# Kernel tuning notes

Measured on AMD Instinct MI355X. Metric: run time of the kernel, lower is better.

## Reference

```python
import jax, jax.numpy as jnp
import numpy as np

B, C, CW = 64, 862, 512
F_BINS = CW // 2 + 1          # 257 rfft bins -> embedding in_features
D_MODEL, N_HEADS, D_FF, N_LAYERS = 256, 16, 512, 3
EPS = 1e-5


def setup_inputs() -> dict:
    key = jax.random.key(0)
    ks = jax.random.split(key, 12)
    s = 0.02
    return {
        'x_re': jax.random.normal(ks[0], (B, C, F_BINS), jnp.float32),
        'x_im': jax.random.normal(ks[1], (B, C, F_BINS), jnp.float32),
        # complex embedding Linear(F_BINS, D_MODEL): weight [D_MODEL, F_BINS], bias [D_MODEL]
        'emb_Wre': jax.random.normal(ks[2], (D_MODEL, F_BINS), jnp.float32) * s,
        'emb_Wim': jax.random.normal(ks[3], (D_MODEL, F_BINS), jnp.float32) * s,
        'emb_bre': jax.random.normal(ks[4], (D_MODEL,), jnp.float32) * s,
        'emb_bim': jax.random.normal(ks[5], (D_MODEL,), jnp.float32) * s,
        # per-layer FFN weights (stacked over layers)
        'W1': jax.random.normal(ks[6], (N_LAYERS, D_FF, D_MODEL), jnp.float32) * s,
        'b1': jnp.zeros((N_LAYERS, D_FF), jnp.float32),
        'W2': jax.random.normal(ks[7], (N_LAYERS, D_MODEL, D_FF), jnp.float32) * s,
        'b2': jnp.zeros((N_LAYERS, D_MODEL), jnp.float32),
        # per-layer BatchNorm affine params (attn norm and ffn norm)
        'gamma1': jnp.ones((N_LAYERS, D_MODEL), jnp.float32),
        'beta1': jnp.zeros((N_LAYERS, D_MODEL), jnp.float32),
        'gamma2': jnp.ones((N_LAYERS, D_MODEL), jnp.float32),
        'beta2': jnp.zeros((N_LAYERS, D_MODEL), jnp.float32),
    }


def _batchnorm(x, g, b):
    # Transpose(1,2) + BatchNorm1d(d_model) + Transpose(1,2): normalize each
    # feature (last axis) over (batch, seq) with batch statistics (training mode).
    m = x.mean(axis=(0, 1))
    v = x.var(axis=(0, 1))  # biased, matching torch normalization
    return (x - m) * jax.lax.rsqrt(v + EPS) * g + b


def _encoder_layer(y, Wff1, bff1, Wff2, bff2, g1, be1, g2, be2):
    # y: [2b, c, d] -- real half stacked over imag half along dim 0
    scale = float(D_MODEL // N_HEADS) ** -0.5
    b = y.shape[0] // 2
    # _MultiheadAttention: q = src, k = flip(src, dims=[1,2]), v = src (no projections applied)
    k = jnp.flip(y, axis=(1, 2))
    q_re, q_im = y[:b], y[b:]
    k_re, k_im = k[:b], k[b:]
    v_re = y[:b]
    v_im = y[:b]  # faithful to source: both halves use v[:bs//2]
    asr = scale * (q_re * k_re - q_im * k_im)
    asi = scale * (q_re * k_im - q_im * k_re)  # minus, as written in source
    o_re = asr * v_re - asi * v_im
    o_im = asr * v_im + asi * v_re
    out = jnp.concatenate([o_re, o_im], axis=0)  # [2b, c, d]
    # transpose(1,2).contiguous().view(bs, -1, d_model): a data shuffle, kept faithfully
    out = jnp.swapaxes(out, 1, 2).reshape(out.shape[0], out.shape[1], out.shape[2])
    src = y + out                       # residual (dropout = 0)
    src = _batchnorm(src, g1, be1)      # post-norm (pre_norm=False)
    ff = jnp.einsum('bcd,fd->bcf', src, Wff1) + bff1
    ff = jax.nn.gelu(ff, approximate=False)
    ff = jnp.einsum('bcf,df->bcd', ff, Wff2) + bff2
    src = src + ff
    src = _batchnorm(src, g2, be2)
    return src


def reference(x_re, x_im, emb_Wre, emb_Wim, emb_bre, emb_bim,
              W1, b1, W2, b2, gamma1, beta1, gamma2, beta2):
    # complex Linear embedding: (x_re + i x_im) @ (Wre + i Wim)^T + (bre + i bim)
    y_re = x_re @ emb_Wre.T - x_im @ emb_Wim.T + emb_bre
    y_im = x_re @ emb_Wim.T + x_im @ emb_Wre.T + emb_bim
    y = jnp.concatenate([y_re, y_im], axis=0)  # [2b, c, d_model]
    for i in range(N_LAYERS):
        y = _encoder_layer(y, W1[i], b1[i], W2[i], b2[i],
                           gamma1[i], beta1[i], gamma2[i], beta2[i])
    b = x_re.shape[0]
    # torch.view_as_complex(stack([y[:b], y[b:]], -1)) -> return real/imag stacked
    return jnp.stack([y[:b], y[b:]], axis=-1)  # [b, c, d_model, 2]
```

## Files before the change

kernel.cpp:

```cpp
#include <hip/hip_runtime.h>
#include <hip/hip_bf16.h>
#include <math.h>

#define BB   64
#define CC   862
#define FB   257
#define DM   256
#define DFF  512
#define NIMG 128
#define ROWS_RE (BB*CC)
#define ROWS_ALL (NIMG*CC)
#define NELEM ((long)ROWS_ALL*DM)

typedef __bf16 bf16x8 __attribute__((ext_vector_type(8)));
typedef float  f32x4  __attribute__((ext_vector_type(4)));

__global__ __launch_bounds__(256) void k_wcvt(const float* __restrict__ W1,
                                              const float* __restrict__ W2,
                                              __bf16* __restrict__ W1b,
                                              __bf16* __restrict__ W2b) {
  long i = ((long)blockIdx.x * 256 + threadIdx.x) * 4;
  const long N1 = 3L * DFF * DM;
  const float* src;
  __bf16* dst;
  if (i < N1) { src = W1 + i; dst = W1b + i; }
  else        { src = W2 + (i - N1); dst = W2b + (i - N1); }
  float4 x = *(const float4*)src;
  dst[0] = (__bf16)x.x; dst[1] = (__bf16)x.y;
  dst[2] = (__bf16)x.z; dst[3] = (__bf16)x.w;
}

__global__ void k_init(double* __restrict__ stats, float* __restrict__ ss) {
  int t = threadIdx.x;
  stats[t] = 0.0;
  if (t < 256) { ss[t] = 1.0f; ss[DM + t] = 0.0f; }
}

#define KE 544
#define PE 552

__global__ __launch_bounds__(256) void k_wemb(const float* __restrict__ Wre,
                                              const float* __restrict__ Wim,
                                              __bf16* __restrict__ Wb) {
  int n = blockIdx.x;
  int d = n & 255;
  bool im = (n >= 256);
  const float* Wa = im ? Wim : Wre;
  const float* Wc = im ? Wre : Wim;
  float sgn = im ? 1.0f : -1.0f;
  for (int k = threadIdx.x; k < KE; k += 256) {
    float v;
    if (k < 257)      v = Wa[(long)d * FB + k];
    else if (k < 514) v = sgn * Wc[(long)d * FB + (k - 257)];
    else              v = 0.0f;
    Wb[(long)n * KE + k] = (__bf16)v;
  }
}

__global__ __launch_bounds__(256, 4) void k_embm(
    const float* __restrict__ xr, const float* __restrict__ xi,
    const __bf16* __restrict__ Wb,
    const float* __restrict__ bre, const float* __restrict__ bim,
    float* __restrict__ A) {
  __shared__ __bf16 sA[32 * PE];
  int t = threadIdx.x;
  int lane = t & 63;
  int w = t >> 6;
  int half = lane >> 4;
  int l16 = lane & 15;
  long row0 = (long)blockIdx.x * 32;

  for (int idx = t; idx < 32 * 30; idx += 256) {
    int r = idx / 30, j = idx - r * 30;
    sA[r * PE + 514 + j] = (__bf16)0.f;
  }
  for (int idx = t; idx < 32 * 257; idx += 256) {
    int r = idx / 257, f = idx - r * 257;
    long g = (row0 + r) * FB + f;
    sA[r * PE + f]       = (__bf16)xr[g];
    sA[r * PE + 257 + f] = (__bf16)xi[g];
  }
  __syncthreads();

  int n0 = w * 128;
  f32x4 acc[2][8];
#pragma unroll
  for (int mt = 0; mt < 2; mt++)
#pragma unroll
    for (int j = 0; j < 8; j++) acc[mt][j] = (f32x4){0.f, 0.f, 0.f, 0.f};

#pragma unroll 1
  for (int kt = 0; kt < 17; kt++) {
    int kb = kt * 32 + half * 8;
    bf16x8 a[2];
#pragma unroll
    for (int mt = 0; mt < 2; mt++)
      a[mt] = *(const bf16x8*)&sA[(mt * 16 + l16) * PE + kb];
#pragma unroll
    for (int j = 0; j < 8; j++) {
      bf16x8 bfr = *(const bf16x8*)&Wb[(long)(n0 + j * 16 + l16) * KE + kb];
#pragma unroll
      for (int mt = 0; mt < 2; mt++)
        acc[mt][j] = __builtin_amdgcn_mfma_f32_16x16x32_bf16(a[mt], bfr, acc[mt][j], 0, 0, 0);
    }
  }

#pragma unroll
  for (int j = 0; j < 8; j++) {
    int n = n0 + j * 16 + l16;
    int d = n & 255;
    float bv = (n < 256) ? bre[d] : bim[d];
    long rbase = (n < 256) ? 0L : (long)ROWS_RE;
#pragma unroll
    for (int mt = 0; mt < 2; mt++)
#pragma unroll
      for (int r = 0; r < 4; r++) {
        int m = mt * 16 + half * 4 + r;
        A[(row0 + m + rbase) * DM + d] = acc[mt][j][r] + bv;
      }
  }
}

__global__ __launch_bounds__(256) void k_attn(const float* __restrict__ A,
                                              const float* __restrict__ ss,
                                              float* __restrict__ T) {
  __shared__ float ore[32][33];
  __shared__ float oim[32][33];
  __shared__ float ssc[256];
  __shared__ float ssh[256];
  int tx = threadIdx.x;
  int ty = threadIdx.y;
  int t = ty * 32 + tx;
  ssc[t] = ss[t];
  ssh[t] = ss[DM + t];
  __syncthreads();

  int c0 = blockIdx.x * 32;
  int d0 = blockIdx.y * 32;
  int b  = blockIdx.z;
  const long base_re = (long)b * CC * DM;
  const long base_im = (long)(b + BB) * CC * DM;
  int d = d0 + tx;
  int kd = DM - 1 - d;
  float scq = ssc[d], shq = ssh[d];
  float sck = ssc[kd], shk = ssh[kd];
#pragma unroll
  for (int q = 0; q < 4; q++) {
    int cl = ty + 8 * q;
    int c = c0 + cl;
    if (c < CC) {
      float qr = fmaf(A[base_re + (long)c * DM + d], scq, shq);
      float qi = fmaf(A[base_im + (long)c * DM + d], scq, shq);
      float kr = fmaf(A[base_re + (long)(CC - 1 - c) * DM + kd], sck, shk);
      float ki = fmaf(A[base_im + (long)(CC - 1 - c) * DM + kd], sck, shk);
      float asr = 0.25f * (qr * kr - qi * ki);
      float asi = 0.25f * (qr * ki - qi * kr);
      ore[cl][tx] = (asr - asi) * qr;
      oim[cl][tx] = (asr + asi) * qr;
    }
  }
  __syncthreads();
#pragma unroll
  for (int q = 0; q < 4; q++) {
    int dl = ty + 8 * q;
    int dd = d0 + dl;
    int c = c0 + tx;
    if (c < CC) {
      long flat = (long)dd * CC + c;
      int dp = (int)(flat & 255);
      float sc = ssc[dp], sh = ssh[dp];
      T[base_re + flat] = fmaf(A[base_re + flat], sc, sh) + ore[tx][dl];
      T[base_im + flat] = fmaf(A[base_im + flat], sc, sh) + oim[tx][dl];
    }
  }
}

__global__ __launch_bounds__(256) void k_bnstats(const float* __restrict__ P,
                                                 double* __restrict__ stats) {
  int d = threadIdx.x;
  long row0 = (long)blockIdx.x * 128;
  double s = 0.0, s2 = 0.0;
  for (int r = 0; r < 128; r++) {
    float x = P[(row0 + r) * DM + d];
    s += (double)x;
    s2 += (double)x * (double)x;
  }
  atomicAdd(&stats[d], s);
  atomicAdd(&stats[DM + d], s2);
}

__global__ void k_finalize(double* __restrict__ stats,
                           const float* __restrict__ g, const float* __restrict__ be,
                           float* __restrict__ ss) {
  int d = threadIdx.x;
  double n = (double)ROWS_ALL;
  double m = stats[d] / n;
  double v = stats[DM + d] / n - m * m;
  float inv = (float)(1.0 / sqrt(v + 1e-5));
  float sc = g[d] * inv;
  ss[d] = sc;
  ss[DM + d] = be[d] - (float)m * sc;
  stats[d] = 0.0;
  stats[DM + d] = 0.0;
}

__global__ __launch_bounds__(256) void k_bnfinal(const float* __restrict__ A,
                                                 const float* __restrict__ ss,
                                                 float* __restrict__ out) {
  long gid = (long)blockIdx.x * 256 + threadIdx.x;
  int d = (int)(gid & 255);
  long bc = gid >> 8;
  float sc = ss[d], sh = ss[DM + d];
  float re = A[bc * DM + d];
  float im = A[(bc + (long)ROWS_RE) * DM + d];
  float2 o;
  o.x = fmaf(re, sc, sh);
  o.y = fmaf(im, sc, sh);
  ((float2*)out)[gid] = o;
}

#define PS2 268
#define PH4 132

__global__ __launch_bounds__(512, 4) void k_ffm(
    const float* __restrict__ P, const float* __restrict__ ss,
    const __bf16* __restrict__ W1b, const float* __restrict__ b1,
    const __bf16* __restrict__ W2b, const float* __restrict__ b2,
    float* __restrict__ Out, double* __restrict__ stats) {
  __shared__ __bf16 sS[64 * PS2];
  __shared__ __bf16 sH[64 * PH4];
  int t = threadIdx.x;
  int lane = t & 63;
  int w = t >> 6;
  int half = lane >> 4;
  int l16 = lane & 15;
  long row0 = (long)blockIdx.x * 64;

  {
    const float4* Pv = (const float4*)(P + row0 * DM);
    const float4* scv = (const float4*)ss;
    const float4* shv = (const float4*)(ss + DM);
#pragma unroll
    for (int i = 0; i < 8; i++) {
      int v = t + i * 512;
      int r = v >> 6, k4 = v & 63;
      float4 x = Pv[(long)r * 64 + k4];
      float4 sc = scv[k4];
      float4 sh = shv[k4];
      x.x = fmaf(x.x, sc.x, sh.x);
      x.y = fmaf(x.y, sc.y, sh.y);
      x.z = fmaf(x.z, sc.z, sh.z);
      x.w = fmaf(x.w, sc.w, sh.w);
      __bf16* dst = &sS[r * PS2 + k4 * 4];
      dst[0] = (__bf16)x.x; dst[1] = (__bf16)x.y;
      dst[2] = (__bf16)x.z; dst[3] = (__bf16)x.w;
    }
  }
  __syncthreads();

  int n2 = w * 32;
  f32x4 acc2[4][2];
#pragma unroll
  for (int mt = 0; mt < 4; mt++)
#pragma unroll
    for (int j = 0; j < 2; j++) acc2[mt][j] = (f32x4){0.f, 0.f, 0.f, 0.f};

#pragma unroll 1
  for (int q = 0; q < 4; q++) {
    if (q > 0) __syncthreads();

    f32x4 acc[4];
#pragma unroll
    for (int mt = 0; mt < 4; mt++) acc[mt] = (f32x4){0.f, 0.f, 0.f, 0.f};

#pragma unroll 2
    for (int kt = 0; kt < 8; kt++) {
      int kb = kt * 32 + half * 8;
      bf16x8 a[4];
#pragma unroll
      for (int mt = 0; mt < 4; mt++)
        a[mt] = *(const bf16x8*)&sS[(mt * 16 + l16) * PS2 + kb];
      bf16x8 bfr = *(const bf16x8*)&W1b[(long)(q * 128 + w * 16 + l16) * DM + kb];
#pragma unroll
      for (int mt = 0; mt < 4; mt++)
        acc[mt] = __builtin_amdgcn_mfma_f32_16x16x32_bf16(a[mt], bfr, acc[mt], 0, 0, 0);
    }

    {
      int fl = w * 16 + l16;
      float b1v = b1[q * 128 + fl];
#pragma unroll
      for (int mt = 0; mt < 4; mt++)
#pragma unroll
        for (int r = 0; r < 4; r++) {
          float x = acc[mt][r] + b1v;
          float u = x * (0.7978845608f + 0.0356774081f * x * x);
          float e = __expf(-2.0f * u);
          float g = x * __builtin_amdgcn_rcpf(1.0f + e);
          int m = mt * 16 + half * 4 + r;
          sH[m * PH4 + fl] = (__bf16)g;
        }
    }
    __syncthreads();

#pragma unroll 2
    for (int kt = 0; kt < 4; kt++) {
      int kb = kt * 32 + half * 8;
      bf16x8 a[4];
#pragma unroll
      for (int mt = 0; mt < 4; mt++)
        a[mt] = *(const bf16x8*)&sH[(mt * 16 + l16) * PH4 + kb];
#pragma unroll
      for (int j = 0; j < 2; j++) {
        bf16x8 bfr = *(const bf16x8*)&W2b[(long)(n2 + j * 16 + l16) * DFF + q * 128 + kb];
#pragma unroll
        for (int mt = 0; mt < 4; mt++)
          acc2[mt][j] = __builtin_amdgcn_mfma_f32_16x16x32_bf16(a[mt], bfr, acc2[mt][j], 0, 0, 0);
      }
    }
  }

  {
#pragma unroll
    for (int j = 0; j < 2; j++) {
      int d = n2 + j * 16 + l16;
      float b2v = b2[d];
      float sc = ss[d], sh = ss[DM + d];
      float s = 0.f, s2 = 0.f;
#pragma unroll
      for (int mt = 0; mt < 4; mt++)
#pragma unroll
        for (int r = 0; r < 4; r++) {
          int m = mt * 16 + half * 4 + r;
          long idx = (row0 + m) * DM + d;
          float vv = fmaf(P[idx], sc, sh) + acc2[mt][j][r] + b2v;
          Out[idx] = vv;
          s += vv;
          s2 += vv * vv;
        }
      s  += __shfl_xor(s, 16);  s  += __shfl_xor(s, 32);
      s2 += __shfl_xor(s2, 16); s2 += __shfl_xor(s2, 32);
      if (half == 0) {
        atomicAdd(&stats[d], (double)s);
        atomicAdd(&stats[DM + d], (double)s2);
      }
    }
  }
}

extern "C" void kernel_launch(void* const* d_in, const int* in_sizes, int n_in,
                              void* d_out, int out_size, void* d_ws, size_t ws_size,
                              hipStream_t stream) {
  const float* xr  = (const float*)d_in[0];
  const float* xi  = (const float*)d_in[1];
  const float* Wre = (const float*)d_in[2];
  const float* Wim = (const float*)d_in[3];
  const float* bre = (const float*)d_in[4];
  const float* bim = (const float*)d_in[5];
  const float* W1  = (const float*)d_in[6];
  const float* b1  = (const float*)d_in[7];
  const float* W2  = (const float*)d_in[8];
  const float* b2  = (const float*)d_in[9];
  const float* g1  = (const float*)d_in[10];
  const float* be1 = (const float*)d_in[11];
  const float* g2  = (const float*)d_in[12];
  const float* be2 = (const float*)d_in[13];

  float* A = (float*)d_ws;
  double* stats = (double*)((char*)d_ws + (size_t)NELEM * 4);
  float* ss = (float*)(stats + 512);
  __bf16* W1b = (__bf16*)(ss + 512);
  __bf16* W2b = W1b + 3L * DFF * DM;
  float* T = (float*)d_out;
  __bf16* Wb = (__bf16*)d_out;

  k_wemb<<<512, 256, 0, stream>>>(Wre, Wim, Wb);
  k_wcvt<<<768, 256, 0, stream>>>(W1, W2, W1b, W2b);
  k_init<<<1, 512, 0, stream>>>(stats, ss);
  k_embm<<<ROWS_RE / 32, 256, 0, stream>>>(xr, xi, Wb, bre, bim, A);

  for (int l = 0; l < 3; l++) {
    k_attn<<<dim3(27, 8, 64), dim3(32, 8), 0, stream>>>(A, ss, T);
    k_bnstats<<<862, 256, 0, stream>>>(T, stats);
    k_finalize<<<1, 256, 0, stream>>>(stats, g1 + l * DM, be1 + l * DM, ss);
    k_ffm<<<ROWS_ALL / 64, 512, 0, stream>>>(T, ss,
                                             W1b + (long)l * DFF * DM, b1 + l * DFF,
                                             W2b + (long)l * DFF * DM, b2 + l * DM,
                                             A, stats);
    k_finalize<<<1, 256, 0, stream>>>(stats, g2 + l * DM, be2 + l * DM, ss);
    if (l == 2) {
      k_bnfinal<<<ROWS_RE * DM / 256, 256, 0, stream>>>(A, ss, (float*)d_out);
    }
  }
}
```

Measured before the change: 1.215 ms.

## Switch FFN kernel to 32x32x16 MFMA tiles with two hidden-dim halves

Rewrites the fused FFN kernel to use 32x32x16 bf16 MFMA instructions instead of 16x16x32. The hidden dimension is now processed in two chunks of 256 rather than four of 128, which enlarges the shared hidden buffer and halves the number of block-wide barriers. Each wave computes 64 rows x 32 columns per chunk with fewer A/B fragment loads per MFMA, aiming at better reuse and MFMA throughput. In exchange, the larger LDS footprint and more accumulator registers may reduce occupancy.

```diff
diff --git a/kernel.cpp b/kernel.cpp
--- a/kernel.cpp
+++ b/kernel.cpp
@@ -14,6 +14,7 @@
 
 typedef __bf16 bf16x8 __attribute__((ext_vector_type(8)));
 typedef float  f32x4  __attribute__((ext_vector_type(4)));
+typedef float  f32x16 __attribute__((ext_vector_type(16)));
 
 __global__ __launch_bounds__(256) void k_wcvt(const float* __restrict__ W1,
                                               const float* __restrict__ W2,
@@ -220,7 +221,7 @@
 }
 
 #define PS2 268
-#define PH4 132
+#define PH2 260
 
 __global__ __launch_bounds__(512, 4) void k_ffm(
     const float* __restrict__ P, const float* __restrict__ ss,
@@ -228,12 +229,12 @@
     const __bf16* __restrict__ W2b, const float* __restrict__ b2,
     float* __restrict__ Out, double* __restrict__ stats) {
   __shared__ __bf16 sS[64 * PS2];
-  __shared__ __bf16 sH[64 * PH4];
+  __shared__ __bf16 sH[64 * PH2];
   int t = threadIdx.x;
   int lane = t & 63;
   int w = t >> 6;
-  int half = lane >> 4;
-  int l16 = lane & 15;
+  int hi = lane >> 5;
+  int l32 = lane & 31;
   long row0 = (long)blockIdx.x * 64;
 
   {
@@ -258,92 +259,83 @@
   }
   __syncthreads();
 
-  int n2 = w * 32;
-  f32x4 acc2[4][2];
-#pragma unroll
-  for (int mt = 0; mt < 4; mt++)
-#pragma unroll
-    for (int j = 0; j < 2; j++) acc2[mt][j] = (f32x4){0.f, 0.f, 0.f, 0.f};
+  f32x16 acc2[2];
+#pragma unroll
+  for (int mt = 0; mt < 2; mt++)
+#pragma unroll
+    for (int r = 0; r < 16; r++) acc2[mt][r] = 0.f;
 
 #pragma unroll 1
-  for (int q = 0; q < 4; q++) {
-    if (q > 0) __syncthreads();
-
-    f32x4 acc[4];
-#pragma unroll
-    for (int mt = 0; mt < 4; mt++) acc[mt] = (f32x4){0.f, 0.f, 0.f, 0.f};
-
+  for (int hf = 0; hf < 2; hf++) {
+    if (hf == 1) __syncthreads();
+
+    f32x16 acc1[2];
+#pragma unroll
+    for (int mt = 0; mt < 2; mt++)
+#pragma unroll
+      for (int r = 0; r < 16; r++) acc1[mt][r] = 0.f;
+
+    const __bf16* w1row = W1b + (long)(hf * 256 + w * 32 + l32) * DM;
 #pragma unroll 2
-    for (int kt = 0; kt < 8; kt++) {
-      int kb = kt * 32 + half * 8;
-      bf16x8 a[4];
-#pragma unroll
-      for (int mt = 0; mt < 4; mt++)
-        a[mt] = *(const bf16x8*)&sS[(mt * 16 + l16) * PS2 + kb];
-      bf16x8 bfr = *(const bf16x8*)&W1b[(long)(q * 128 + w * 16 + l16) * DM + kb];
-#pragma unroll
-      for (int mt = 0; mt < 4; mt++)
-        acc[mt] = __builtin_amdgcn_mfma_f32_16x16x32_bf16(a[mt], bfr, acc[mt], 0, 0, 0);
+    for (int kt = 0; kt < 16; kt++) {
+      int kb = kt * 16 + hi * 8;
+      bf16x8 a0 = *(const bf16x8*)&sS[l32 * PS2 + kb];
+      bf16x8 a1 = *(const bf16x8*)&sS[(32 + l32) * PS2 + kb];
+      bf16x8 bfr = *(const bf16x8*)&w1row[kb];
+      acc1[0] = __builtin_amdgcn_mfma_f32_32x32x16_bf16(a0, bfr, acc1[0], 0, 0, 0);
+      acc1[1] = __builtin_amdgcn_mfma_f32_32x32x16_bf16(a1, bfr, acc1[1], 0, 0, 0);
     }
 
     {
-      int fl = w * 16 + l16;
-      float b1v = b1[q * 128 + fl];
-#pragma unroll
-      for (int mt = 0; mt < 4; mt++)
-#pragma unroll
-        for (int r = 0; r < 4; r++) {
-          float x = acc[mt][r] + b1v;
+      int fl = w * 32 + l32;
+      float b1v = b1[hf * 256 + fl];
+#pragma unroll
+      for (int mt = 0; mt < 2; mt++)
+#pragma unroll
+        for (int r = 0; r < 16; r++) {
+          float x = acc1[mt][r] + b1v;
           float u = x * (0.7978845608f + 0.0356774081f * x * x);
           float e = __expf(-2.0f * u);
           float g = x * __builtin_amdgcn_rcpf(1.0f + e);
-          int m = mt * 16 + half * 4 + r;
-          sH[m * PH4 + fl] = (__bf16)g;
+          int m = mt * 32 + (r & 3) + 8 * (r >> 2) + 4 * hi;
+          sH[m * PH2 + fl] = (__bf16)g;
         }
     }
     __syncthreads();
 
+    const __bf16* w2row = W2b + (long)(w * 32 + l32) * DFF + hf * 256;
 #pragma unroll 2
-    for (int kt = 0; kt < 4; kt++) {
-      int kb = kt * 32 + half * 8;
-      bf16x8 a[4];
-#pragma unroll
-      for (int mt = 0; mt < 4; mt++)
-        a[mt] = *(const bf16x8*)&sH[(mt * 16 + l16) * PH4 + kb];
-#pragma unroll
-      for (int j = 0; j < 2; j++) {
-        bf16x8 bfr = *(const bf16x8*)&W2b[(long)(n2 + j * 16 + l16) * DFF + q * 128 + kb];
-#pragma unroll
-        for (int mt = 0; mt < 4; mt++)
-          acc2[mt][j] = __builtin_amdgcn_mfma_f32_16x16x32_bf16(a[mt], bfr, acc2[mt][j], 0, 0, 0);
+    for (int kt = 0; kt < 16; kt++) {
+      int kb = kt * 16 + hi * 8;
+      bf16x8 a0 = *(const bf16x8*)&sH[l32 * PH2 + kb];
+      bf16x8 a1 = *(const bf16x8*)&sH[(32 + l32) * PH2 + kb];
+      bf16x8 bfr = *(const bf16x8*)&w2row[kb];
+      acc2[0] = __builtin_amdgcn_mfma_f32_32x32x16_bf16(a0, bfr, acc2[0], 0, 0, 0);
+      acc2[1] = __builtin_amdgcn_mfma_f32_32x32x16_bf16(a1, bfr, acc2[1], 0, 0, 0);
+    }
+  }
+
+  {
+    int d = w * 32 + l32;
+    float b2v = b2[d];
+    float sc = ss[d], sh = ss[DM + d];
+    float s = 0.f, s2 = 0.f;
+#pragma unroll
+    for (int mt = 0; mt < 2; mt++)
+#pragma unroll
+      for (int r = 0; r < 16; r++) {
+        int m = mt * 32 + (r & 3) + 8 * (r >> 2) + 4 * hi;
+        long idx = (row0 + m) * DM + d;
+        float vv = fmaf(P[idx], sc, sh) + acc2[mt][r] + b2v;
+        Out[idx] = vv;
+        s += vv;
+        s2 += vv * vv;
       }
-    }
-  }
-
-  {
-#pragma unroll
-    for (int j = 0; j < 2; j++) {
-      int d = n2 + j * 16 + l16;
-      float b2v = b2[d];
-      float sc = ss[d], sh = ss[DM + d];
-      float s = 0.f, s2 = 0.f;
-#pragma unroll
-      for (int mt = 0; mt < 4; mt++)
-#pragma unroll
-        for (int r = 0; r < 4; r++) {
-          int m = mt * 16 + half * 4 + r;
-          long idx = (row0 + m) * DM + d;
-          float vv = fmaf(P[idx], sc, sh) + acc2[mt][j][r] + b2v;
-          Out[idx] = vv;
-          s += vv;
-          s2 += vv * vv;
-        }
-      s  += __shfl_xor(s, 16);  s  += __shfl_xor(s, 32);
-      s2 += __shfl_xor(s2, 16); s2 += __shfl_xor(s2, 32);
-      if (half == 0) {
-        atomicAdd(&stats[d], (double)s);
-        atomicAdd(&stats[DM + d], (double)s2);
-      }
+    s  += __shfl_xor(s, 32);
+    s2 += __shfl_xor(s2, 32);
+    if (hi == 0) {
+      atomicAdd(&stats[d], (double)s);
+      atomicAdd(&stats[DM + d], (double)s2);
     }
   }
 }
```

After: 1.188 ms. 1.02x faster.
